# Kernel tuning notes

Measured on AMD Instinct MI355X. Metric: run time of the kernel, lower is better.

## Reference

```python
import math
import jax, jax.numpy as jnp
import numpy as np

C, H, W, N = 128, 64, 64, 32


def setup_inputs() -> dict:
    key = jax.random.key(0)
    k = jax.random.split(key, 6)
    std = 0.02
    return {
        "x": jax.random.normal(k[0], (N, C, H, W), dtype=jnp.float32),
        # p_3: 1x1 conv, weight [out=C, in=3C]
        "w3": jax.random.normal(k[1], (C, 3 * C), dtype=jnp.float32) * std,
        "p5_w": jax.random.normal(k[2], (1, 1, H, W), dtype=jnp.float32) * std,
        # p_6: conv (3,1), dilation (3,1), weight [O=C, I=C, 3, 1]
        "w6": jax.random.normal(k[3], (C, C, 3, 1), dtype=jnp.float32) * std,
        "p8_w": jax.random.normal(k[4], (1, C, 1, 1), dtype=jnp.float32) * std,
        "p12_w": jax.random.normal(k[5], (1, 1, 3, H, 1), dtype=jnp.float32) * std,
    }


def reference(x, w3, p5_w, w6, p8_w, p12_w):
    n, c, h, w = x.shape
    # F.unfold(x, (1,3), dilation=(1,2), padding=(0,2)) -> taps at w-2, w, w+2 (zero padded)
    xp = jnp.pad(x, ((0, 0), (0, 0), (0, 0), (2, 2)))
    t1 = jnp.stack([xp[..., 0:w], xp[..., 2:w + 2], xp[..., 4:w + 4]], axis=2)  # [n,c,3,h,w]
    t2 = t1.max(axis=2)                                                          # [n,c,h,w]
    # p_3: 1x1 conv over 3c channels
    t3 = jnp.einsum('nkhw,ok->nohw', t1.reshape(n, c * 3, h, w), w3)            # [n,c,h,w]
    t4 = jnp.maximum(t3[:, :, None], t1)                                         # [n,c,3,h,w]
    t5 = p5_w * t2
    # p_6: (3,1) conv, dilation (3,1), padding (3,0) -> same spatial size
    t6 = jax.lax.conv_general_dilated(
        t5, w6, window_strides=(1, 1), padding=((3, 3), (0, 0)),
        rhs_dilation=(3, 1), dimension_numbers=('NCHW', 'OIHW', 'NCHW'))         # [n,c,h,w]
    t7 = jnp.maximum(x, t6)
    t8 = p8_w * t7
    # bmm: [n,c,hw] x [n,hw,3c] -> [n,c,3c]
    t9 = jnp.einsum('ncp,nkp->nck', t8.reshape(n, c, h * w),
                    t1.reshape(n, c * 3, h * w)) / math.sqrt(h * w)
    t10 = t7[:, :, None] + t4                                                    # [n,c,3,h,w]
    t11 = jnp.maximum(t6[:, :, None], t10)                                       # [n,c,3,h,w]
    t12 = p12_w * t11
    # bmm: [n,hw,3c] x [n,3c,c] -> [n,hw,c]
    t13 = jnp.einsum('nkp,nck->npc', t12.reshape(n, c * 3, h * w), t9) / math.sqrt(c * 3)
    return t13.reshape(n, h, w, c).transpose(0, 3, 1, 2)                         # [n,c,h,w]
```

## Files before the change

kernel.cpp:

```cpp
#include <hip/hip_runtime.h>

#define C_   128
#define P_   4096
#define K3   384
#define CP   (C_*P_)
#define NB_  32
#define PR_  4480

typedef __attribute__((ext_vector_type(8))) short short8;
typedef __attribute__((ext_vector_type(4))) short short4v;
typedef __attribute__((ext_vector_type(4))) float f32x4;

__device__ __forceinline__ short f2bf(float f) {
  union { float f; unsigned u; } v; v.f = f;
  unsigned r = v.u + 0x7fffu + ((v.u >> 16) & 1u);
  return (short)(r >> 16);
}
__device__ __forceinline__ float bf2f(short b) {
  union { unsigned u; float f; } v; v.u = ((unsigned)(unsigned short)b) << 16;
  return v.f;
}
__device__ __forceinline__ void gl_lds16(const void* g, void* l) {
  __builtin_amdgcn_global_load_lds(
      (const __attribute__((address_space(1))) unsigned int*)g,
      (__attribute__((address_space(3))) unsigned int*)l, 16, 0, 0);
}

__global__ __launch_bounds__(256) void prep_kernel(const float* __restrict__ w3,
                                                   const float* __restrict__ w6,
                                                   short* __restrict__ w3p,
                                                   short* __restrict__ w6p) {
  int idx = blockIdx.x * 256 + threadIdx.x;
  int m = idx / K3, kp = idx - m * K3;
  int j = kp >> 7, c = kp & 127;
  w3p[idx] = f2bf(w3[m * K3 + c * 3 + j]);
  w6p[idx] = f2bf(w6[m * K3 + c * 3 + j]);
}

__global__ __launch_bounds__(256) void xk_kernel(const float* __restrict__ x,
                                                 const float* __restrict__ p5,
                                                 short* __restrict__ xb,
                                                 short* __restrict__ xT,
                                                 short* __restrict__ t5p) {
  int b = blockIdx.x;
  int pt = b & 63, ct = (b >> 6) & 1, n = b >> 7;
  int p0 = pt * 64, c0 = ct * 64;
  const float* xn = x + (size_t)n * CP;
  short* xbn = xb + (size_t)n * CP;
  short* xTn = xT + (size_t)n * CP;
  short* t5n = t5p + (size_t)n * PR_ * C_;
  __shared__ short Ls[64][68];
  int tid = threadIdx.x;
#pragma unroll
  for (int it = 0; it < 4; ++it) {
    int fid = tid + it * 256;
    int i = fid >> 4, j4 = fid & 15;
    f32x4 v = *(const f32x4*)(xn + (c0 + i) * P_ + p0 + j4 * 4);
    short4v s;
#pragma unroll
    for (int r = 0; r < 4; ++r) s[r] = f2bf(v[r]);
    *(short4v*)(xbn + (c0 + i) * P_ + p0 + j4 * 4) = s;
    *(short4v*)(&Ls[i][j4 * 4]) = s;
  }
  __syncthreads();
#pragma unroll
  for (int it = 0; it < 4; ++it) {
    int oid = tid + it * 256;
    int pr = oid >> 4, cg = oid & 15, cb = cg * 4;
    float p5v = p5[p0 + pr];
    short4v a, t5v;
#pragma unroll
    for (int r = 0; r < 4; ++r) {
      a[r] = Ls[cb + r][pr];
      float m = bf2f(a[r]);
      float l = (pr >= 2) ? bf2f(Ls[cb + r][pr - 2]) : 0.0f;
      float rr = (pr < 62) ? bf2f(Ls[cb + r][pr + 2]) : 0.0f;
      t5v[r] = f2bf(p5v * fmaxf(fmaxf(l, m), rr));
    }
    *(short4v*)(xTn + (p0 + pr) * C_ + c0 + cb) = a;
    *(short4v*)(t5n + (size_t)(192 + p0 + pr) * C_ + c0 + cb) = t5v;
  }
}

__global__ __launch_bounds__(256, 4) void g12_kernel(const short* __restrict__ w3p,
                                                     const short* __restrict__ w6p,
                                                     const short* __restrict__ t5p,
                                                     const short* __restrict__ xT,
                                                     short* __restrict__ t3T,
                                                     short* __restrict__ t6T,
                                                     short* __restrict__ t7T) {
  int blk = blockIdx.x;
  int role = blk & 1;
  int b = blk >> 1;
  int n = b >> 5, pt = b & 31, p0 = pt * 128;
  int tid = threadIdx.x, lane = tid & 63, wv = tid >> 6;
  int wm = (wv & 1) * 64, wp = (wv >> 1) * 64;
  const short* Ap = role ? w3p : w6p;
  const short* xTn = xT + (size_t)n * CP;
  const short* t5n = t5p + (size_t)n * PR_ * C_;
  __shared__ __align__(16) short As[2][4][128][8];
  __shared__ __align__(16) short Bs[2][4][128][8];
  f32x4 acc[4][4] = {};
  short8 bm[2];

  auto stageA = [&](int ks, int bf) {
    int k0 = (ks % 3) * 128 + (ks / 3) * 32;
#pragma unroll
    for (int it = 0; it < 2; ++it) {
      int slot = tid + it * 256;
      int q = slot >> 7, m = slot & 127;
      gl_lds16(Ap + m * K3 + k0 + q * 8, &As[bf][q][m][0]);
    }
  };
  auto stageB0 = [&](int ks, int bf) {
    int jr = ks % 3, cb = ks / 3;
    const short* src = t5n + (size_t)(jr * 192 + p0) * C_ + cb * 32;
#pragma unroll
    for (int it = 0; it < 2; ++it) {
      int slot = tid + it * 256;
      int q = slot >> 7, pc = slot & 127;
      gl_lds16(src + (size_t)pc * C_ + q * 8, &Bs[bf][q][pc][0]);
    }
  };
  auto loadB1 = [&](int ks) {
    int jr = ks % 3;
#pragma unroll
    for (int it = 0; it < 2; ++it) {
      int slot = tid + it * 256;
      int q = slot & 3, pc = slot >> 2;
      int p = p0 + pc;
      int c0k = (ks / 3) * 32 + q * 8;
      int d = 2 * (jr - 1);
      int prc = min(max(p + d, 0), P_ - 1);
      bm[it] = *(const short8*)(xTn + (size_t)prc * C_ + c0k);
    }
  };
  auto writeB1 = [&](int ks, int bf) {
    int jr = ks % 3;
#pragma unroll
    for (int it = 0; it < 2; ++it) {
      int slot = tid + it * 256;
      int q = slot & 3, pc = slot >> 2;
      int p = p0 + pc;
      int d = 2 * (jr - 1);
      int wd = (p & 63) + d;
      short8 zero = {};
      short8 v = bm[it];
      if (!(wd >= 0 && wd < 64)) v = zero;
      *(short8*)(&Bs[bf][q][pc][0]) = v;
    }
  };

  stageA(0, 0);
  if (role) { loadB1(0); writeB1(0, 0); } else stageB0(0, 0);
  __syncthreads();
#pragma unroll 2
  for (int ks = 0; ks < 12; ++ks) {
    int cur = ks & 1, nxt = cur ^ 1;
    if (ks < 11) {
      stageA(ks + 1, nxt);
      if (role) loadB1(ks + 1); else stageB0(ks + 1, nxt);
    }
    int row = lane & 15, q = lane >> 4;
    short8 a[4], bb[4];
#pragma unroll
    for (int im = 0; im < 4; ++im) a[im] = *(const short8*)(&As[cur][q][wm + im * 16 + row][0]);
#pragma unroll
    for (int ip = 0; ip < 4; ++ip) bb[ip] = *(const short8*)(&Bs[cur][q][wp + ip * 16 + row][0]);
#pragma unroll
    for (int im = 0; im < 4; ++im)
#pragma unroll
      for (int ip = 0; ip < 4; ++ip)
        acc[im][ip] = __builtin_amdgcn_mfma_f32_16x16x32_bf16(a[im], bb[ip], acc[im][ip], 0, 0, 0);
    if (ks < 11 && role) writeB1(ks + 1, nxt);
    __syncthreads();
  }
  int col = lane & 15, rq = lane >> 4;
  if (role) {
    short* t3Tn = t3T + (size_t)n * CP;
#pragma unroll
    for (int im = 0; im < 4; ++im)
#pragma unroll
      for (int ip = 0; ip < 4; ++ip) {
        int m0 = wm + im * 16 + rq * 4;
        int p = p0 + wp + ip * 16 + col;
        short4v s;
#pragma unroll
        for (int r = 0; r < 4; ++r) s[r] = f2bf(acc[im][ip][r]);
        *(short4v*)(t3Tn + (size_t)p * C_ + m0) = s;
      }
  } else {
    short* t6Tn = t6T + (size_t)n * CP;
    short* t7Tn = t7T + (size_t)n * CP;
#pragma unroll
    for (int im = 0; im < 4; ++im)
#pragma unroll
      for (int ip = 0; ip < 4; ++ip) {
        int m0 = wm + im * 16 + rq * 4;
        int p = p0 + wp + ip * 16 + col;
        short4v ax = *(const short4v*)(xTn + (size_t)p * C_ + m0);
        short4v s6, s7;
#pragma unroll
        for (int r = 0; r < 4; ++r) {
          float t6v = acc[im][ip][r];
          float t7v = fmaxf(bf2f(ax[r]), t6v);
          s6[r] = f2bf(t6v);
          s7[r] = f2bf(t7v);
        }
        *(short4v*)(t6Tn + (size_t)p * C_ + m0) = s6;
        *(short4v*)(t7Tn + (size_t)p * C_ + m0) = s7;
      }
  }
}

__global__ __launch_bounds__(256, 4) void g3_kernel(const short* __restrict__ xb,
                                                    const short* __restrict__ t7T,
                                                    float* __restrict__ t9) {
  int blk = blockIdx.x;
  int nb = blk % 3;
  int tmp = blk / 3;
  int n = tmp & 31, sk = tmp >> 5;
  int d = 2 * (nb - 1);
  int tid = threadIdx.x, lane = tid & 63, wv = tid >> 6;
  int wm = (wv & 1) * 64, wp = (wv >> 1) * 64;
  const short* xbn = xb + (size_t)n * CP;
  const short* t7n = t7T + (size_t)n * CP;
  __shared__ __align__(16) short As[2][4][128][8];
  __shared__ __align__(16) short Bs[2][4][128][8];
  f32x4 acc[4][4] = {};
  short8 av[2], bv[2];

  auto loadAB = [&](int ks) {
    int pp0 = sk * 512 + ks * 32;
#pragma unroll
    for (int it = 0; it < 2; ++it) {
      int slot = tid + it * 256;
      int q = slot >> 7, rr = slot & 127;
      int pb = pp0 + q * 8;
      const int* src = (const int*)(xbn + rr * P_ + pb + d);
      union { int i[4]; short8 s; } u;
#pragma unroll
      for (int t = 0; t < 4; ++t) u.i[t] = src[t];
      av[it] = u.s;
      const short* bp = t7n + (size_t)pb * C_ + rr;
      short8 w;
#pragma unroll
      for (int j = 0; j < 8; ++j) w[j] = bp[j * C_];
      bv[it] = w;
    }
  };
  auto writeAB = [&](int ks, int bf) {
    int pp0 = sk * 512 + ks * 32;
#pragma unroll
    for (int it = 0; it < 2; ++it) {
      int slot = tid + it * 256;
      int q = slot >> 7, rr = slot & 127;
      int pb = pp0 + q * 8;
      short8 v = av[it];
      int w0 = pb & 63;
      if (nb == 0) { if (w0 == 0) { v[0] = 0; v[1] = 0; } }
      else if (nb == 2) { if (w0 == 56) { v[6] = 0; v[7] = 0; } }
      *(short8*)(&As[bf][q][rr][0]) = v;
      *(short8*)(&Bs[bf][q][rr][0]) = bv[it];
    }
  };

  loadAB(0);
  writeAB(0, 0);
  __syncthreads();
#pragma unroll 2
  for (int ks = 0; ks < 16; ++ks) {
    int cur = ks & 1, nxt = cur ^ 1;
    if (ks < 15) loadAB(ks + 1);
    int row = lane & 15, q = lane >> 4;
    short8 a[4], bb[4];
#pragma unroll
    for (int im = 0; im < 4; ++im) a[im] = *(const short8*)(&As[cur][q][wm + im * 16 + row][0]);
#pragma unroll
    for (int ip = 0; ip < 4; ++ip) bb[ip] = *(const short8*)(&Bs[cur][q][wp + ip * 16 + row][0]);
#pragma unroll
    for (int im = 0; im < 4; ++im)
#pragma unroll
      for (int ip = 0; ip < 4; ++ip)
        acc[im][ip] = __builtin_amdgcn_mfma_f32_16x16x32_bf16(a[im], bb[ip], acc[im][ip], 0, 0, 0);
    if (ks < 15) writeAB(ks + 1, nxt);
    __syncthreads();
  }
  int col = lane & 15, rq = lane >> 4;
  float* t9n = t9 + (size_t)n * (K3 * C_);
#pragma unroll
  for (int im = 0; im < 4; ++im)
#pragma unroll
    for (int ip = 0; ip < 4; ++ip)
#pragma unroll
      for (int r = 0; r < 4; ++r) {
        int kp = nb * 128 + wm + im * 16 + rq * 4 + r;
        int c = wp + ip * 16 + col;
        atomicAdd(&t9n[(size_t)kp * C_ + c], acc[im][ip][r]);
      }
}

__global__ __launch_bounds__(256) void t9s_kernel(const float* __restrict__ t9,
                                                  const float* __restrict__ p8,
                                                  short* __restrict__ t9b) {
  int b = blockIdx.x;
  int n = b / 6, kt = b - n * 6;
  int k0 = kt * 64;
  const float INV = 1.0f / (64.0f * 19.5959179423f);
  const float* t9n = t9 + (size_t)n * (K3 * C_);
  short* t9bn = t9b + (size_t)n * (C_ * K3);
  __shared__ float L[64][132];
  int tid = threadIdx.x;
#pragma unroll
  for (int it = 0; it < 8; ++it) {
    int s = tid + it * 256;
    int k = s >> 5, c4 = s & 31;
    f32x4 v = *(const f32x4*)(t9n + (size_t)(k0 + k) * C_ + c4 * 4);
    *(f32x4*)(&L[k][c4 * 4]) = v;
  }
  __syncthreads();
#pragma unroll
  for (int it = 0; it < 2; ++it) {
    int s = tid + it * 256;
    int c = s >> 2, kg = s & 3;
    float sc = p8[c] * INV;
    short8 o0, o1;
#pragma unroll
    for (int j = 0; j < 8; ++j) o0[j] = f2bf(L[kg * 16 + j][c] * sc);
#pragma unroll
    for (int j = 0; j < 8; ++j) o1[j] = f2bf(L[kg * 16 + 8 + j][c] * sc);
    short* op = t9bn + (size_t)c * K3 + k0 + kg * 16;
    *(short8*)(op) = o0;
    *(short8*)(op + 8) = o1;
  }
}

__global__ __launch_bounds__(256) void t12k_kernel(const float* __restrict__ p12,
                                                   const short* __restrict__ xT,
                                                   short* __restrict__ t3T,
                                                   short* __restrict__ t6T,
                                                   short* __restrict__ t7T) {
  int idx = blockIdx.x * 256 + threadIdx.x;
  int cg = idx & 15;
  int p  = (idx >> 4) & 4095;
  int n  = idx >> 16;
  size_t base = (size_t)n * CP + (size_t)p * C_ + cg * 8;
  short8 a3 = *(const short8*)(t3T + base);
  short8 a6 = *(const short8*)(t6T + base);
  short8 a7 = *(const short8*)(t7T + base);
  const short* xn = xT + (size_t)n * CP;
  int c0 = cg * 8;
  int h = p >> 6, w = p & 63;
  short8 outv[3];
#pragma unroll
  for (int j = 0; j < 3; ++j) {
    int d = 2 * (j - 1);
    int wd = w + d;
    bool valid = (wd >= 0 && wd < 64);
    int pr = min(max(p + d, 0), P_ - 1);
    short8 ax = *(const short8*)(xn + (size_t)pr * C_ + c0);
    short8 zero = {};
    if (!valid) ax = zero;
    float s12 = p12[j * 64 + h];
    short8 v;
#pragma unroll
    for (int jj = 0; jj < 8; ++jj) {
      float t11 = fmaxf(bf2f(a6[jj]), bf2f(a7[jj]) + fmaxf(bf2f(a3[jj]), bf2f(ax[jj])));
      v[jj] = f2bf(s12 * t11);
    }
    outv[j] = v;
  }
  *(short8*)(t3T + base) = outv[0];
  *(short8*)(t6T + base) = outv[1];
  *(short8*)(t7T + base) = outv[2];
}

__global__ __launch_bounds__(256, 4) void g4_kernel(const short* __restrict__ t9b,
                                                    const short* __restrict__ t12,
                                                    float* __restrict__ out) {
  int b = blockIdx.x;
  int n = b >> 5, pt = b & 31, p0 = pt * 128;
  int tid = threadIdx.x, lane = tid & 63, wv = tid >> 6;
  int wm = (wv & 1) * 64, wp = (wv >> 1) * 64;
  const short* t9n = t9b + (size_t)n * (K3 * C_);
  const size_t SL = (size_t)NB_ * CP;
  __shared__ __align__(16) short As[2][4][128][8];
  __shared__ __align__(16) short Bs[2][4][128][8];
  f32x4 acc[4][4] = {};

  auto stageA = [&](int ks, int bf) {
    int k0 = (ks % 3) * 128 + (ks / 3) * 32;
#pragma unroll
    for (int it = 0; it < 2; ++it) {
      int slot = tid + it * 256;
      int q = slot >> 7, m = slot & 127;
      gl_lds16(t9n + (size_t)m * K3 + k0 + q * 8, &As[bf][q][m][0]);
    }
  };
  auto stageB = [&](int ks, int bf) {
    int j = ks % 3, cb = ks / 3;
    const short* src = t12 + (size_t)j * SL + (size_t)n * CP;
#pragma unroll
    for (int it = 0; it < 2; ++it) {
      int slot = tid + it * 256;
      int q = slot >> 7, pc = slot & 127;
      gl_lds16(src + (size_t)(p0 + pc) * C_ + cb * 32 + q * 8, &Bs[bf][q][pc][0]);
    }
  };

  stageA(0, 0);
  stageB(0, 0);
  __syncthreads();
#pragma unroll 2
  for (int ks = 0; ks < 12; ++ks) {
    int cur = ks & 1, nxt = cur ^ 1;
    if (ks < 11) { stageA(ks + 1, nxt); stageB(ks + 1, nxt); }
    int row = lane & 15, q = lane >> 4;
    short8 a[4], bb[4];
#pragma unroll
    for (int im = 0; im < 4; ++im) a[im] = *(const short8*)(&As[cur][q][wm + im * 16 + row][0]);
#pragma unroll
    for (int ip = 0; ip < 4; ++ip) bb[ip] = *(const short8*)(&Bs[cur][q][wp + ip * 16 + row][0]);
#pragma unroll
    for (int im = 0; im < 4; ++im)
#pragma unroll
      for (int ip = 0; ip < 4; ++ip)
        acc[im][ip] = __builtin_amdgcn_mfma_f32_16x16x32_bf16(a[im], bb[ip], acc[im][ip], 0, 0, 0);
    __syncthreads();
  }
  int col = lane & 15, rq = lane >> 4;
#pragma unroll
  for (int im = 0; im < 4; ++im)
#pragma unroll
    for (int ip = 0; ip < 4; ++ip)
#pragma unroll
      for (int r = 0; r < 4; ++r) {
        int m = wm + im * 16 + rq * 4 + r;
        int p = p0 + wp + ip * 16 + col;
        out[(size_t)n * CP + m * P_ + p] = acc[im][ip][r];
      }
}

extern "C" void kernel_launch(void* const* d_in, const int* in_sizes, int n_in,
                              void* d_out, int out_size, void* d_ws, size_t ws_size,
                              hipStream_t stream) {
  const float* x   = (const float*)d_in[0];
  const float* w3  = (const float*)d_in[1];
  const float* p5  = (const float*)d_in[2];
  const float* w6  = (const float*)d_in[3];
  const float* p8  = (const float*)d_in[4];
  const float* p12 = (const float*)d_in[5];
  float* out = (float*)d_out;

  char* ws = (char*)d_ws;
  const size_t RB = (size_t)NB_ * CP * 2;
  size_t off = 256;
  short* xb  = (short*)(ws + off); off += RB;
  short* xT  = (short*)(ws + off); off += RB;
  short* t3T = (short*)(ws + off); off += RB;
  short* t6T = (short*)(ws + off); off += RB;
  short* t7T = (short*)(ws + off); off += RB;
  float* t9  = (float*)(ws + off); off += (size_t)NB_ * K3 * C_ * 4;
  short* w3p = (short*)(ws + off); off += 49152 * 2;
  short* w6p = (short*)(ws + off); off += 49152 * 2;
  short* t9b = xb;
  short* t5p = (short*)out;

  prep_kernel<<<192, 256, 0, stream>>>(w3, w6, w3p, w6p);
  hipMemsetAsync(t5p, 0, (size_t)NB_ * PR_ * C_ * 2, stream);
  xk_kernel<<<4096, 256, 0, stream>>>(x, p5, xb, xT, t5p);
  g12_kernel<<<2048, 256, 0, stream>>>(w3p, w6p, t5p, xT, t3T, t6T, t7T);
  hipMemsetAsync(t9, 0, (size_t)NB_ * K3 * C_ * sizeof(float), stream);
  g3_kernel<<<768, 256, 0, stream>>>(xb, t7T, t9);
  t9s_kernel<<<192, 256, 0, stream>>>(t9, p8, t9b);
  t12k_kernel<<<8192, 256, 0, stream>>>(p12, xT, t3T, t6T, t7T);
  g4_kernel<<<1024, 256, 0, stream>>>(t9b, t3T, out);
}
```

Measured before the change: 415.3 us.

## Issue loads two k-steps ahead with fine-grained vmcnt waits in the GEMM kernels

Both MFMA GEMM loops now prefetch two k-steps ahead into the double buffer, with explicit s_waitcnt vmcnt and raw s_barrier in place of __syncthreads, so global-to-LDS loads overlap more with compute. The t3 role's B operand now goes through direct global_load_lds with clamped indices, and a later LDS patch zeroes the out-of-range taps, replacing the earlier register load plus LDS write. The vmcnt(4) count assumes exactly four outstanding loads per stage, so any change in how many loads a stage issues would break correctness.

```diff
diff --git a/kernel.cpp b/kernel.cpp
--- a/kernel.cpp
+++ b/kernel.cpp
@@ -101,7 +101,6 @@
   __shared__ __align__(16) short As[2][4][128][8];
   __shared__ __align__(16) short Bs[2][4][128][8];
   f32x4 acc[4][4] = {};
-  short8 bm[2];
 
   auto stageA = [&](int ks, int bf) {
     int k0 = (ks % 3) * 128 + (ks / 3) * 32;
@@ -112,68 +111,70 @@
       gl_lds16(Ap + m * K3 + k0 + q * 8, &As[bf][q][m][0]);
     }
   };
-  auto stageB0 = [&](int ks, int bf) {
+  auto stageB = [&](int ks, int bf) {
     int jr = ks % 3, cb = ks / 3;
-    const short* src = t5n + (size_t)(jr * 192 + p0) * C_ + cb * 32;
+    if (role) {
+      int d = 2 * (jr - 1);
+#pragma unroll
+      for (int it = 0; it < 2; ++it) {
+        int slot = tid + it * 256;
+        int q = slot >> 7, pc = slot & 127;
+        int prc = min(max(p0 + pc + d, 0), P_ - 1);
+        gl_lds16(xTn + (size_t)prc * C_ + cb * 32 + q * 8, &Bs[bf][q][pc][0]);
+      }
+    } else {
+      const short* src = t5n + (size_t)(jr * 192 + p0) * C_ + cb * 32;
+#pragma unroll
+      for (int it = 0; it < 2; ++it) {
+        int slot = tid + it * 256;
+        int q = slot >> 7, pc = slot & 127;
+        gl_lds16(src + (size_t)pc * C_ + q * 8, &Bs[bf][q][pc][0]);
+      }
+    }
+  };
+  auto patchB1 = [&](int ks, int bf) {
+    int jr = ks % 3;
+    if (jr == 1) return;
+    int d = 2 * (jr - 1);
 #pragma unroll
     for (int it = 0; it < 2; ++it) {
       int slot = tid + it * 256;
       int q = slot >> 7, pc = slot & 127;
-      gl_lds16(src + (size_t)pc * C_ + q * 8, &Bs[bf][q][pc][0]);
-    }
-  };
-  auto loadB1 = [&](int ks) {
-    int jr = ks % 3;
-#pragma unroll
-    for (int it = 0; it < 2; ++it) {
-      int slot = tid + it * 256;
-      int q = slot & 3, pc = slot >> 2;
-      int p = p0 + pc;
-      int c0k = (ks / 3) * 32 + q * 8;
-      int d = 2 * (jr - 1);
-      int prc = min(max(p + d, 0), P_ - 1);
-      bm[it] = *(const short8*)(xTn + (size_t)prc * C_ + c0k);
-    }
-  };
-  auto writeB1 = [&](int ks, int bf) {
-    int jr = ks % 3;
-#pragma unroll
-    for (int it = 0; it < 2; ++it) {
-      int slot = tid + it * 256;
-      int q = slot & 3, pc = slot >> 2;
-      int p = p0 + pc;
-      int d = 2 * (jr - 1);
-      int wd = (p & 63) + d;
-      short8 zero = {};
-      short8 v = bm[it];
-      if (!(wd >= 0 && wd < 64)) v = zero;
-      *(short8*)(&Bs[bf][q][pc][0]) = v;
-    }
-  };
-
-  stageA(0, 0);
-  if (role) { loadB1(0); writeB1(0, 0); } else stageB0(0, 0);
-  __syncthreads();
-#pragma unroll 2
+      int wd = (pc & 63) + d;
+      if (!(wd >= 0 && wd < 64)) {
+        short8 zero = {};
+        *(short8*)(&Bs[bf][q][pc][0]) = zero;
+      }
+    }
+  };
+
+  stageA(0, 0); stageB(0, 0);
+  stageA(1, 1); stageB(1, 1);
+  int row = lane & 15, qk = lane >> 4;
   for (int ks = 0; ks < 12; ++ks) {
-    int cur = ks & 1, nxt = cur ^ 1;
-    if (ks < 11) {
-      stageA(ks + 1, nxt);
-      if (role) loadB1(ks + 1); else stageB0(ks + 1, nxt);
-    }
-    int row = lane & 15, q = lane >> 4;
+    int cur = ks & 1;
+    if (ks < 11) asm volatile("s_waitcnt vmcnt(4)" ::: "memory");
+    else         asm volatile("s_waitcnt vmcnt(0)" ::: "memory");
+    if (role) {
+      patchB1(ks, cur);
+      asm volatile("s_waitcnt lgkmcnt(0)" ::: "memory");
+    }
+    __builtin_amdgcn_s_barrier();
+    __builtin_amdgcn_sched_barrier(0);
     short8 a[4], bb[4];
 #pragma unroll
-    for (int im = 0; im < 4; ++im) a[im] = *(const short8*)(&As[cur][q][wm + im * 16 + row][0]);
-#pragma unroll
-    for (int ip = 0; ip < 4; ++ip) bb[ip] = *(const short8*)(&Bs[cur][q][wp + ip * 16 + row][0]);
+    for (int im = 0; im < 4; ++im) a[im] = *(const short8*)(&As[cur][qk][wm + im * 16 + row][0]);
+#pragma unroll
+    for (int ip = 0; ip < 4; ++ip) bb[ip] = *(const short8*)(&Bs[cur][qk][wp + ip * 16 + row][0]);
+    asm volatile("s_waitcnt lgkmcnt(0)" ::: "memory");
+    __builtin_amdgcn_sched_barrier(0);
 #pragma unroll
     for (int im = 0; im < 4; ++im)
 #pragma unroll
       for (int ip = 0; ip < 4; ++ip)
         acc[im][ip] = __builtin_amdgcn_mfma_f32_16x16x32_bf16(a[im], bb[ip], acc[im][ip], 0, 0, 0);
-    if (ks < 11 && role) writeB1(ks + 1, nxt);
-    __syncthreads();
+    __builtin_amdgcn_s_barrier();
+    if (ks < 10) { stageA(ks + 2, cur); stageB(ks + 2, cur); }
   }
   int col = lane & 15, rq = lane >> 4;
   if (role) {
@@ -408,25 +409,29 @@
     }
   };
 
-  stageA(0, 0);
-  stageB(0, 0);
-  __syncthreads();
-#pragma unroll 2
+  stageA(0, 0); stageB(0, 0);
+  stageA(1, 1); stageB(1, 1);
+  int row = lane & 15, qk = lane >> 4;
   for (int ks = 0; ks < 12; ++ks) {
-    int cur = ks & 1, nxt = cur ^ 1;
-    if (ks < 11) { stageA(ks + 1, nxt); stageB(ks + 1, nxt); }
-    int row = lane & 15, q = lane >> 4;
+    int cur = ks & 1;
+    if (ks < 11) asm volatile("s_waitcnt vmcnt(4)" ::: "memory");
+    else         asm volatile("s_waitcnt vmcnt(0)" ::: "memory");
+    __builtin_amdgcn_s_barrier();
+    __builtin_amdgcn_sched_barrier(0);
     short8 a[4], bb[4];
 #pragma unroll
-    for (int im = 0; im < 4; ++im) a[im] = *(const short8*)(&As[cur][q][wm + im * 16 + row][0]);
-#pragma unroll
-    for (int ip = 0; ip < 4; ++ip) bb[ip] = *(const short8*)(&Bs[cur][q][wp + ip * 16 + row][0]);
+    for (int im = 0; im < 4; ++im) a[im] = *(const short8*)(&As[cur][qk][wm + im * 16 + row][0]);
+#pragma unroll
+    for (int ip = 0; ip < 4; ++ip) bb[ip] = *(const short8*)(&Bs[cur][qk][wp + ip * 16 + row][0]);
+    asm volatile("s_waitcnt lgkmcnt(0)" ::: "memory");
+    __builtin_amdgcn_sched_barrier(0);
 #pragma unroll
     for (int im = 0; im < 4; ++im)
 #pragma unroll
       for (int ip = 0; ip < 4; ++ip)
         acc[im][ip] = __builtin_amdgcn_mfma_f32_16x16x32_bf16(a[im], bb[ip], acc[im][ip], 0, 0, 0);
-    __syncthreads();
+    __builtin_amdgcn_s_barrier();
+    if (ks < 10) { stageA(ks + 2, cur); stageB(ks + 2, cur); }
   }
   int col = lane & 15, rq = lane >> 4;
 #pragma unroll
```

New measurement: 429.4 us. 1.03x slower.
